# Kernel tuning notes

Measured on AMD Instinct MI355X. Metric: run time of the kernel, lower is better.

## Reference

```python
import jax, jax.numpy as jnp
import numpy as np

B, T, E = 65536, 50, 10


def _glorot(key, shape):
    fan_in, fan_out = shape[0], shape[-1]
    limit = np.sqrt(6.0 / (fan_in + fan_out))
    return jax.random.uniform(key, shape, jnp.float32, -limit, limit)


def setup_inputs() -> dict:
    key = jax.random.key(0)
    ks = jax.random.split(key, 20)
    inp = {
        "gru_hidden_state_inputs": jax.random.normal(ks[0], (B, T, E), jnp.float32),
        "attention_s": jax.random.uniform(ks[1], (B, T, E), jnp.float32),
        # initial hidden state: GlorotUniform(shape=(1, E)) as in the TF code
        "h0": _glorot(ks[2], (1, E)),
    }
    # R_t gate (sigmoid): input_w (with bias), hidden_w (no bias), Dense_sigmoid (with bias)
    inp["Wi_r"] = _glorot(ks[3], (E, E)); inp["bi_r"] = jnp.zeros((E,), jnp.float32)
    inp["Wh_r"] = _glorot(ks[4], (E, E))
    inp["Ws_r"] = _glorot(ks[5], (E, E)); inp["bs_r"] = jnp.zeros((E,), jnp.float32)
    # Z_t gate (sigmoid)
    inp["Wi_z"] = _glorot(ks[6], (E, E)); inp["bi_z"] = jnp.zeros((E,), jnp.float32)
    inp["Wh_z"] = _glorot(ks[7], (E, E))
    inp["Ws_z"] = _glorot(ks[8], (E, E)); inp["bs_z"] = jnp.zeros((E,), jnp.float32)
    # H_t_next candidate (tanh)
    inp["Wi_h"] = _glorot(ks[9], (E, E)); inp["bi_h"] = jnp.zeros((E,), jnp.float32)
    inp["Wh_h"] = _glorot(ks[10], (E, E))
    inp["Wt_h"] = _glorot(ks[11], (E, E)); inp["bt_h"] = jnp.zeros((E,), jnp.float32)
    return inp


def reference(gru_hidden_state_inputs, attention_s, h0,
              Wi_r, bi_r, Wh_r, Ws_r, bs_r,
              Wi_z, bi_z, Wh_z, Ws_z, bs_z,
              Wi_h, bi_h, Wh_h, Wt_h, bt_h):
    b, t, e = gru_hidden_state_inputs.shape
    h = jnp.broadcast_to(h0, (b, e))  # TF broadcasts the (1,E) init against the batch
    # scan over time: xs are [T, B, E]
    xs = (jnp.swapaxes(gru_hidden_state_inputs, 0, 1),
          jnp.swapaxes(attention_s, 0, 1))

    def step(h, xa):
        x_t, a_t = xa
        # note: each gate has an EXTRA dense layer (Dense_sigmoid / Dense_tanh are Dense layers)
        r = jax.nn.sigmoid((x_t @ Wi_r + bi_r + h @ Wh_r) @ Ws_r + bs_r)
        z = jax.nn.sigmoid((x_t @ Wi_z + bi_z + h @ Wh_z) @ Ws_z + bs_z)
        hc = jnp.tanh((x_t @ Wi_h + bi_h + (h * z) @ Wh_h) @ Wt_h + bt_h)
        Ra = a_t * r
        h_next = (1.0 - Ra) * h + Ra * hc
        return h_next, None

    h_final, _ = jax.lax.scan(step, h, xs)
    return h_final
```

## Files before the change

### kernel.cpp

```cpp
#include <hip/hip_runtime.h>

#define EDIM 10
#define TDIM 50
#define BATCH 65536
#define CWN 640

__device__ float g_cw[CWN];

typedef const __attribute__((address_space(4))) float cfloat;

__device__ __forceinline__ float fast_sigmoid(float x) {
    float e = __expf(-x);
    return __builtin_amdgcn_rcpf(1.0f + e);
}
__device__ __forceinline__ float fast_tanh(float x) {
    float e = __expf(2.0f * x);
    return 1.0f - 2.0f * __builtin_amdgcn_rcpf(e + 1.0f);
}

__global__ void collapse_weights(
    const float* __restrict__ Wi_r, const float* __restrict__ bi_r,
    const float* __restrict__ Wh_r, const float* __restrict__ Ws_r, const float* __restrict__ bs_r,
    const float* __restrict__ Wi_z, const float* __restrict__ bi_z,
    const float* __restrict__ Wh_z, const float* __restrict__ Ws_z, const float* __restrict__ bs_z,
    const float* __restrict__ Wi_h, const float* __restrict__ bi_h,
    const float* __restrict__ Wh_h, const float* __restrict__ Wt_h, const float* __restrict__ bt_h)
{
    for (int s = threadIdx.x; s < 630; s += 256) {
        int g, kind, k, e;
        if (s < 30)       { kind = 0; g = s / 10;      k = 0;                e = s % 10; }
        else if (s < 330) { kind = 1; int q = s - 30;  g = q / 100; k = (q % 100) / 10; e = q % 10; }
        else              { kind = 2; int q = s - 330; g = q / 100; k = (q % 100) / 10; e = q % 10; }
        const float* Wi = (g == 0) ? Wi_r : (g == 1) ? Wi_z : Wi_h;
        const float* Wh = (g == 0) ? Wh_r : (g == 1) ? Wh_z : Wh_h;
        const float* Ws = (g == 0) ? Ws_r : (g == 1) ? Ws_z : Wt_h;
        const float* bi = (g == 0) ? bi_r : (g == 1) ? bi_z : bi_h;
        const float* bs = (g == 0) ? bs_r : (g == 1) ? bs_z : bt_h;
        float v = 0.0f;
        if (kind == 0) {
            v = bs[e];
            #pragma unroll
            for (int j = 0; j < 10; j++) v += bi[j] * Ws[j * 10 + e];
        } else {
            const float* M = (kind == 1) ? Wi : Wh;
            #pragma unroll
            for (int j = 0; j < 10; j++) v += M[k * 10 + j] * Ws[j * 10 + e];
        }
        g_cw[s] = v;
    }
}

__global__ __launch_bounds__(256, 1) void augru_main(
    const float* __restrict__ x_all, const float* __restrict__ a_all,
    const float* __restrict__ h0,
    float* __restrict__ out)
{
    const int row = blockIdx.x * 256 + threadIdx.x;

    cfloat* cw = (cfloat*)(uintptr_t)(const float*)g_cw;

    const float2* xp = (const float2*)(x_all + (size_t)row * (TDIM * EDIM));
    const float2* ap = (const float2*)(a_all + (size_t)row * (TDIM * EDIM));

    float h[10];
    #pragma unroll
    for (int j = 0; j < 10; j++) h[j] = h0[j];

    float xc[10], ac[10];
    #pragma unroll
    for (int i = 0; i < 5; i++) {
        float2 v = xp[i]; xc[2 * i] = v.x; xc[2 * i + 1] = v.y;
        float2 u = ap[i]; ac[2 * i] = u.x; ac[2 * i + 1] = u.y;
    }

    int sofs = 0;

    #pragma unroll 1
    for (int t = 0; t < TDIM; t++) {
        asm volatile("" : "+s"(sofs));
        cfloat* w = cw + sofs;

        int tn = (t < TDIM - 1) ? (t + 1) : t;
        float xn[10], an[10];
        #pragma unroll
        for (int i = 0; i < 5; i++) {
            float2 v = xp[tn * 5 + i]; xn[2 * i] = v.x; xn[2 * i + 1] = v.y;
            float2 u = ap[tn * 5 + i]; an[2 * i] = u.x; an[2 * i + 1] = u.y;
        }

        float ur[10], uz[10], uh[10];
        #pragma unroll
        for (int j = 0; j < 10; j++) {
            ur[j] = w[j]; uz[j] = w[10 + j]; uh[j] = w[20 + j];
        }

        #pragma unroll
        for (int k = 0; k < 10; k++) {
            float xk = xc[k];
            #pragma unroll
            for (int j = 0; j < 10; j++) ur[j] = fmaf(xk, w[30 + k * 10 + j], ur[j]);
        }
        #pragma unroll
        for (int k = 0; k < 10; k++) {
            float xk = xc[k];
            #pragma unroll
            for (int j = 0; j < 10; j++) uz[j] = fmaf(xk, w[130 + k * 10 + j], uz[j]);
        }
        #pragma unroll
        for (int k = 0; k < 10; k++) {
            float hk = h[k];
            #pragma unroll
            for (int j = 0; j < 10; j++) ur[j] = fmaf(hk, w[330 + k * 10 + j], ur[j]);
        }
        #pragma unroll
        for (int k = 0; k < 10; k++) {
            float hk = h[k];
            #pragma unroll
            for (int j = 0; j < 10; j++) uz[j] = fmaf(hk, w[430 + k * 10 + j], uz[j]);
        }
        #pragma unroll
        for (int k = 0; k < 10; k++) {
            float xk = xc[k];
            #pragma unroll
            for (int j = 0; j < 10; j++) uh[j] = fmaf(xk, w[230 + k * 10 + j], uh[j]);
        }

        float hz[10];
        #pragma unroll
        for (int j = 0; j < 10; j++) hz[j] = h[j] * fast_sigmoid(uz[j]);

        #pragma unroll
        for (int k = 0; k < 10; k++) {
            float hk = hz[k];
            #pragma unroll
            for (int j = 0; j < 10; j++) uh[j] = fmaf(hk, w[530 + k * 10 + j], uh[j]);
        }

        #pragma unroll
        for (int j = 0; j < 10; j++) {
            float r  = fast_sigmoid(ur[j]);
            float hc = fast_tanh(uh[j]);
            float Ra = ac[j] * r;
            h[j] = fmaf(Ra, hc - h[j], h[j]);
        }

        #pragma unroll
        for (int j = 0; j < 10; j++) { xc[j] = xn[j]; ac[j] = an[j]; }
    }

    float2* orow = (float2*)(out + (size_t)row * EDIM);
    #pragma unroll
    for (int i = 0; i < 5; i++) orow[i] = make_float2(h[2 * i], h[2 * i + 1]);
}

extern "C" void kernel_launch(void* const* d_in, const int* in_sizes, int n_in,
                              void* d_out, int out_size, void* d_ws, size_t ws_size,
                              hipStream_t stream) {
    collapse_weights<<<1, 256, 0, stream>>>(
        (const float*)d_in[3],  (const float*)d_in[4],  (const float*)d_in[5],
        (const float*)d_in[6],  (const float*)d_in[7],
        (const float*)d_in[8],  (const float*)d_in[9],  (const float*)d_in[10],
        (const float*)d_in[11], (const float*)d_in[12],
        (const float*)d_in[13], (const float*)d_in[14], (const float*)d_in[15],
        (const float*)d_in[16], (const float*)d_in[17]);
    augru_main<<<BATCH / 256, 256, 0, stream>>>(
        (const float*)d_in[0], (const float*)d_in[1], (const float*)d_in[2],
        (float*)d_out);
}
```

Before: 353.8 us.

## Stage collapsed weights in LDS with padded rows and vector broadcast reads

Moves the collapsed weight matrix from scalar constant loads (s_load through the scalar cache) into shared memory, with each row padded to 12 floats so it can be read with float4/float2 LDS broadcast loads. Before, the weights came in through SGPR scalar loads, which are cheap and uniform. Now every lane issues LDS reads, so LDS instruction traffic and VGPR use go up in exchange for not depending on the scalar cache. The weight offset is also pinned to a VGPR instead of an SGPR.

```diff
diff --git a/kernel.cpp b/kernel.cpp
--- a/kernel.cpp
+++ b/kernel.cpp
@@ -3,11 +3,14 @@
 #define EDIM 10
 #define TDIM 50
 #define BATCH 65536
-#define CWN 640
+#define WPAD 12
+#define WTOT (63 * WPAD)
 
-__device__ float g_cw[CWN];
+__device__ float g_cwp[WTOT];
 
-typedef const __attribute__((address_space(4))) float cfloat;
+#define WROWA(g, k) (((g) * 20 + (k)) * WPAD)
+#define WROWB(g, k) (((g) * 20 + 10 + (k)) * WPAD)
+#define WBIAS(g)    ((60 + (g)) * WPAD)
 
 __device__ __forceinline__ float fast_sigmoid(float x) {
     float e = __expf(-x);
@@ -18,6 +21,28 @@
     return 1.0f - 2.0f * __builtin_amdgcn_rcpf(e + 1.0f);
 }
 
+#define MV_ROW(dst, s, rowptr) do {                                          \
+    const float* rp_ = (rowptr);                                             \
+    float4 w0_ = *(const float4*)(rp_);                                      \
+    float4 w1_ = *(const float4*)(rp_ + 4);                                  \
+    float2 w2_ = *(const float2*)(rp_ + 8);                                  \
+    dst[0] = fmaf((s), w0_.x, dst[0]); dst[1] = fmaf((s), w0_.y, dst[1]);    \
+    dst[2] = fmaf((s), w0_.z, dst[2]); dst[3] = fmaf((s), w0_.w, dst[3]);    \
+    dst[4] = fmaf((s), w1_.x, dst[4]); dst[5] = fmaf((s), w1_.y, dst[5]);    \
+    dst[6] = fmaf((s), w1_.z, dst[6]); dst[7] = fmaf((s), w1_.w, dst[7]);    \
+    dst[8] = fmaf((s), w2_.x, dst[8]); dst[9] = fmaf((s), w2_.y, dst[9]);    \
+} while (0)
+
+#define LD_ROW(dst, rowptr) do {                                             \
+    const float* rp_ = (rowptr);                                             \
+    float4 w0_ = *(const float4*)(rp_);                                      \
+    float4 w1_ = *(const float4*)(rp_ + 4);                                  \
+    float2 w2_ = *(const float2*)(rp_ + 8);                                  \
+    dst[0] = w0_.x; dst[1] = w0_.y; dst[2] = w0_.z; dst[3] = w0_.w;          \
+    dst[4] = w1_.x; dst[5] = w1_.y; dst[6] = w1_.z; dst[7] = w1_.w;          \
+    dst[8] = w2_.x; dst[9] = w2_.y;                                          \
+} while (0)
+
 __global__ void collapse_weights(
     const float* __restrict__ Wi_r, const float* __restrict__ bi_r,
     const float* __restrict__ Wh_r, const float* __restrict__ Ws_r, const float* __restrict__ bs_r,
@@ -26,27 +51,29 @@
     const float* __restrict__ Wi_h, const float* __restrict__ bi_h,
     const float* __restrict__ Wh_h, const float* __restrict__ Wt_h, const float* __restrict__ bt_h)
 {
-    for (int s = threadIdx.x; s < 630; s += 256) {
-        int g, kind, k, e;
-        if (s < 30)       { kind = 0; g = s / 10;      k = 0;                e = s % 10; }
-        else if (s < 330) { kind = 1; int q = s - 30;  g = q / 100; k = (q % 100) / 10; e = q % 10; }
-        else              { kind = 2; int q = s - 330; g = q / 100; k = (q % 100) / 10; e = q % 10; }
-        const float* Wi = (g == 0) ? Wi_r : (g == 1) ? Wi_z : Wi_h;
-        const float* Wh = (g == 0) ? Wh_r : (g == 1) ? Wh_z : Wh_h;
-        const float* Ws = (g == 0) ? Ws_r : (g == 1) ? Ws_z : Wt_h;
-        const float* bi = (g == 0) ? bi_r : (g == 1) ? bi_z : bi_h;
-        const float* bs = (g == 0) ? bs_r : (g == 1) ? bs_z : bt_h;
+    for (int s = threadIdx.x; s < WTOT; s += 256) {
+        int r = s / WPAD, j = s % WPAD;
         float v = 0.0f;
-        if (kind == 0) {
-            v = bs[e];
-            #pragma unroll
-            for (int j = 0; j < 10; j++) v += bi[j] * Ws[j * 10 + e];
-        } else {
-            const float* M = (kind == 1) ? Wi : Wh;
-            #pragma unroll
-            for (int j = 0; j < 10; j++) v += M[k * 10 + j] * Ws[j * 10 + e];
+        if (j < 10) {
+            if (r < 60) {
+                int g = r / 20, kind = (r % 20) / 10, k = r % 10;
+                const float* Ws = (g == 0) ? Ws_r : (g == 1) ? Ws_z : Wt_h;
+                const float* M  = (kind == 0)
+                    ? ((g == 0) ? Wi_r : (g == 1) ? Wi_z : Wi_h)
+                    : ((g == 0) ? Wh_r : (g == 1) ? Wh_z : Wh_h);
+                #pragma unroll
+                for (int jj = 0; jj < 10; jj++) v += M[k * 10 + jj] * Ws[jj * 10 + j];
+            } else {
+                int g = r - 60;
+                const float* Ws = (g == 0) ? Ws_r : (g == 1) ? Ws_z : Wt_h;
+                const float* bi = (g == 0) ? bi_r : (g == 1) ? bi_z : bi_h;
+                const float* bs = (g == 0) ? bs_r : (g == 1) ? bs_z : bt_h;
+                v = bs[j];
+                #pragma unroll
+                for (int jj = 0; jj < 10; jj++) v += bi[jj] * Ws[jj * 10 + j];
+            }
         }
-        g_cw[s] = v;
+        g_cwp[s] = v;
     }
 }
 
@@ -55,9 +82,11 @@
     const float* __restrict__ h0,
     float* __restrict__ out)
 {
+    __shared__ __align__(16) float WL[WTOT];
+    for (int s = threadIdx.x; s < WTOT; s += 256) WL[s] = g_cwp[s];
+    __syncthreads();
+
     const int row = blockIdx.x * 256 + threadIdx.x;
-
-    cfloat* cw = (cfloat*)(uintptr_t)(const float*)g_cw;
 
     const float2* xp = (const float2*)(x_all + (size_t)row * (TDIM * EDIM));
     const float2* ap = (const float2*)(a_all + (size_t)row * (TDIM * EDIM));
@@ -73,12 +102,12 @@
         float2 u = ap[i]; ac[2 * i] = u.x; ac[2 * i + 1] = u.y;
     }
 
-    int sofs = 0;
+    int wofs = 0;
 
     #pragma unroll 1
     for (int t = 0; t < TDIM; t++) {
-        asm volatile("" : "+s"(sofs));
-        cfloat* w = cw + sofs;
+        asm volatile("" : "+v"(wofs));
+        const float* w = (const float*)WL + wofs;
 
         int tn = (t < TDIM - 1) ? (t + 1) : t;
         float xn[10], an[10];
@@ -89,52 +118,27 @@
         }
 
         float ur[10], uz[10], uh[10];
-        #pragma unroll
-        for (int j = 0; j < 10; j++) {
-            ur[j] = w[j]; uz[j] = w[10 + j]; uh[j] = w[20 + j];
-        }
+        LD_ROW(ur, w + WBIAS(0));
+        LD_ROW(uz, w + WBIAS(1));
+        LD_ROW(uh, w + WBIAS(2));
 
         #pragma unroll
-        for (int k = 0; k < 10; k++) {
-            float xk = xc[k];
-            #pragma unroll
-            for (int j = 0; j < 10; j++) ur[j] = fmaf(xk, w[30 + k * 10 + j], ur[j]);
-        }
+        for (int k = 0; k < 10; k++) MV_ROW(ur, xc[k], w + WROWA(0, k));
         #pragma unroll
-        for (int k = 0; k < 10; k++) {
-            float xk = xc[k];
-            #pragma unroll
-            for (int j = 0; j < 10; j++) uz[j] = fmaf(xk, w[130 + k * 10 + j], uz[j]);
-        }
+        for (int k = 0; k < 10; k++) MV_ROW(uz, xc[k], w + WROWA(1, k));
         #pragma unroll
-        for (int k = 0; k < 10; k++) {
-            float hk = h[k];
-            #pragma unroll
-            for (int j = 0; j < 10; j++) ur[j] = fmaf(hk, w[330 + k * 10 + j], ur[j]);
-        }
+        for (int k = 0; k < 10; k++) MV_ROW(ur, h[k],  w + WROWB(0, k));
         #pragma unroll
-        for (int k = 0; k < 10; k++) {
-            float hk = h[k];
-            #pragma unroll
-            for (int j = 0; j < 10; j++) uz[j] = fmaf(hk, w[430 + k * 10 + j], uz[j]);
-        }
+        for (int k = 0; k < 10; k++) MV_ROW(uz, h[k],  w + WROWB(1, k));
         #pragma unroll
-        for (int k = 0; k < 10; k++) {
-            float xk = xc[k];
-            #pragma unroll
-            for (int j = 0; j < 10; j++) uh[j] = fmaf(xk, w[230 + k * 10 + j], uh[j]);
-        }
+        for (int k = 0; k < 10; k++) MV_ROW(uh, xc[k], w + WROWA(2, k));
 
         float hz[10];
         #pragma unroll
         for (int j = 0; j < 10; j++) hz[j] = h[j] * fast_sigmoid(uz[j]);
 
         #pragma unroll
-        for (int k = 0; k < 10; k++) {
-            float hk = hz[k];
-            #pragma unroll
-            for (int j = 0; j < 10; j++) uh[j] = fmaf(hk, w[530 + k * 10 + j], uh[j]);
-        }
+        for (int k = 0; k < 10; k++) MV_ROW(uh, hz[k], w + WROWB(2, k));
 
         #pragma unroll
         for (int j = 0; j < 10; j++) {
```

Result: slower. 367.3 us (+3.8%).

## Hold collapsed weights in registers: hidden weights in VGPRs, input weights via readlane

Applied to the files above, without the earlier changes.

Splits the collapsed weight table into an input/bias part and a hidden part. The hidden-weight matrices are loaded once into a large per-thread register array, and the input weights plus biases are spread across six per-lane registers and broadcast with readlane each step. The aim is to remove the repeated scalar constant loads of weights from the timestep loop. In exchange it sharply raises VGPR usage and adds hundreds of readlane instructions per step on the vector pipe.

```diff
diff --git a/kernel.cpp b/kernel.cpp
--- a/kernel.cpp
+++ b/kernel.cpp
@@ -3,11 +3,9 @@
 #define EDIM 10
 #define TDIM 50
 #define BATCH 65536
-#define CWN 640
-
-__device__ float g_cw[CWN];
-
-typedef const __attribute__((address_space(4))) float cfloat;
+
+__device__ __align__(16) float g_cwA[384];
+__device__ __align__(16) float g_cwB[304];
 
 __device__ __forceinline__ float fast_sigmoid(float x) {
     float e = __expf(-x);
@@ -17,6 +15,11 @@
     float e = __expf(2.0f * x);
     return 1.0f - 2.0f * __builtin_amdgcn_rcpf(e + 1.0f);
 }
+
+#define RL(i) __uint_as_float(__builtin_amdgcn_readlane( \
+                  __float_as_uint(wreg[(i) >> 6]), (i) & 63))
+#define FENCEW() asm volatile("" : "+v"(wreg[0]), "+v"(wreg[1]), "+v"(wreg[2]), \
+    "+v"(wreg[3]), "+v"(wreg[4]), "+v"(wreg[5]))
 
 __global__ void collapse_weights(
     const float* __restrict__ Wi_r, const float* __restrict__ bi_r,
@@ -26,27 +29,35 @@
     const float* __restrict__ Wi_h, const float* __restrict__ bi_h,
     const float* __restrict__ Wh_h, const float* __restrict__ Wt_h, const float* __restrict__ bt_h)
 {
-    for (int s = threadIdx.x; s < 630; s += 256) {
-        int g, kind, k, e;
-        if (s < 30)       { kind = 0; g = s / 10;      k = 0;                e = s % 10; }
-        else if (s < 330) { kind = 1; int q = s - 30;  g = q / 100; k = (q % 100) / 10; e = q % 10; }
-        else              { kind = 2; int q = s - 330; g = q / 100; k = (q % 100) / 10; e = q % 10; }
-        const float* Wi = (g == 0) ? Wi_r : (g == 1) ? Wi_z : Wi_h;
-        const float* Wh = (g == 0) ? Wh_r : (g == 1) ? Wh_z : Wh_h;
-        const float* Ws = (g == 0) ? Ws_r : (g == 1) ? Ws_z : Wt_h;
-        const float* bi = (g == 0) ? bi_r : (g == 1) ? bi_z : bi_h;
-        const float* bs = (g == 0) ? bs_r : (g == 1) ? bs_z : bt_h;
+    for (int s = threadIdx.x; s < 384; s += 256) {
         float v = 0.0f;
-        if (kind == 0) {
-            v = bs[e];
-            #pragma unroll
-            for (int j = 0; j < 10; j++) v += bi[j] * Ws[j * 10 + e];
-        } else {
-            const float* M = (kind == 1) ? Wi : Wh;
-            #pragma unroll
-            for (int j = 0; j < 10; j++) v += M[k * 10 + j] * Ws[j * 10 + e];
-        }
-        g_cw[s] = v;
+        if (s < 300) {
+            int g = s / 100, k = (s % 100) / 10, j = s % 10;
+            const float* Wi = (g == 0) ? Wi_r : (g == 1) ? Wi_z : Wi_h;
+            const float* Ws = (g == 0) ? Ws_r : (g == 1) ? Ws_z : Wt_h;
+            #pragma unroll
+            for (int jj = 0; jj < 10; jj++) v += Wi[k * 10 + jj] * Ws[jj * 10 + j];
+        } else if (s < 330) {
+            int g = (s - 300) / 10, j = (s - 300) % 10;
+            const float* Ws = (g == 0) ? Ws_r : (g == 1) ? Ws_z : Wt_h;
+            const float* bi = (g == 0) ? bi_r : (g == 1) ? bi_z : bi_h;
+            const float* bs = (g == 0) ? bs_r : (g == 1) ? bs_z : bt_h;
+            v = bs[j];
+            #pragma unroll
+            for (int jj = 0; jj < 10; jj++) v += bi[jj] * Ws[jj * 10 + j];
+        }
+        g_cwA[s] = v;
+    }
+    for (int s = threadIdx.x; s < 304; s += 256) {
+        float v = 0.0f;
+        if (s < 300) {
+            int g = s / 100, k = (s % 100) / 10, j = s % 10;
+            const float* Wh = (g == 0) ? Wh_r : (g == 1) ? Wh_z : Wh_h;
+            const float* Ws = (g == 0) ? Ws_r : (g == 1) ? Ws_z : Wt_h;
+            #pragma unroll
+            for (int jj = 0; jj < 10; jj++) v += Wh[k * 10 + jj] * Ws[jj * 10 + j];
+        }
+        g_cwB[s] = v;
     }
 }
 
@@ -55,9 +66,29 @@
     const float* __restrict__ h0,
     float* __restrict__ out)
 {
-    const int row = blockIdx.x * 256 + threadIdx.x;
-
-    cfloat* cw = (cfloat*)(uintptr_t)(const float*)g_cw;
+    const int lane = threadIdx.x & 63;
+    const int row  = blockIdx.x * 256 + threadIdx.x;
+
+    float wreg[6];
+    {
+        int lofs = 0;
+        asm volatile("" : "+v"(lofs));
+        #pragma unroll
+        for (int i = 0; i < 6; i++) wreg[i] = g_cwA[i * 64 + lane + lofs];
+    }
+
+    float Bv[300];
+    {
+        int lofs = 0;
+        asm volatile("" : "+v"(lofs));
+        const float* bp = (const float*)g_cwB + lofs;
+        #pragma unroll
+        for (int i = 0; i < 75; i++) {
+            float4 v = *(const float4*)(bp + 4 * i);
+            Bv[4 * i + 0] = v.x; Bv[4 * i + 1] = v.y;
+            Bv[4 * i + 2] = v.z; Bv[4 * i + 3] = v.w;
+        }
+    }
 
     const float2* xp = (const float2*)(x_all + (size_t)row * (TDIM * EDIM));
     const float2* ap = (const float2*)(a_all + (size_t)row * (TDIM * EDIM));
@@ -73,13 +104,8 @@
         float2 u = ap[i]; ac[2 * i] = u.x; ac[2 * i + 1] = u.y;
     }
 
-    int sofs = 0;
-
     #pragma unroll 1
     for (int t = 0; t < TDIM; t++) {
-        asm volatile("" : "+s"(sofs));
-        cfloat* w = cw + sofs;
-
         int tn = (t < TDIM - 1) ? (t + 1) : t;
         float xn[10], an[10];
         #pragma unroll
@@ -89,40 +115,45 @@
         }
 
         float ur[10], uz[10], uh[10];
+        FENCEW();
         #pragma unroll
         for (int j = 0; j < 10; j++) {
-            ur[j] = w[j]; uz[j] = w[10 + j]; uh[j] = w[20 + j];
-        }
-
+            ur[j] = RL(300 + j); uz[j] = RL(310 + j); uh[j] = RL(320 + j);
+        }
+
+        FENCEW();
         #pragma unroll
         for (int k = 0; k < 10; k++) {
             float xk = xc[k];
             #pragma unroll
-            for (int j = 0; j < 10; j++) ur[j] = fmaf(xk, w[30 + k * 10 + j], ur[j]);
-        }
+            for (int j = 0; j < 10; j++) ur[j] = fmaf(xk, RL(0 + k * 10 + j), ur[j]);
+        }
+        FENCEW();
         #pragma unroll
         for (int k = 0; k < 10; k++) {
             float xk = xc[k];
             #pragma unroll
-            for (int j = 0; j < 10; j++) uz[j] = fmaf(xk, w[130 + k * 10 + j], uz[j]);
-        }
+            for (int j = 0; j < 10; j++) uz[j] = fmaf(xk, RL(100 + k * 10 + j), uz[j]);
+        }
+        FENCEW();
+        #pragma unroll
+        for (int k = 0; k < 10; k++) {
+            float xk = xc[k];
+            #pragma unroll
+            for (int j = 0; j < 10; j++) uh[j] = fmaf(xk, RL(200 + k * 10 + j), uh[j]);
+        }
+
         #pragma unroll
         for (int k = 0; k < 10; k++) {
             float hk = h[k];
             #pragma unroll
-            for (int j = 0; j < 10; j++) ur[j] = fmaf(hk, w[330 + k * 10 + j], ur[j]);
+            for (int j = 0; j < 10; j++) ur[j] = fmaf(hk, Bv[0 + k * 10 + j], ur[j]);
         }
         #pragma unroll
         for (int k = 0; k < 10; k++) {
             float hk = h[k];
             #pragma unroll
-            for (int j = 0; j < 10; j++) uz[j] = fmaf(hk, w[430 + k * 10 + j], uz[j]);
-        }
-        #pragma unroll
-        for (int k = 0; k < 10; k++) {
-            float xk = xc[k];
-            #pragma unroll
-            for (int j = 0; j < 10; j++) uh[j] = fmaf(xk, w[230 + k * 10 + j], uh[j]);
+            for (int j = 0; j < 10; j++) uz[j] = fmaf(hk, Bv[100 + k * 10 + j], uz[j]);
         }
 
         float hz[10];
@@ -133,7 +164,7 @@
         for (int k = 0; k < 10; k++) {
             float hk = hz[k];
             #pragma unroll
-            for (int j = 0; j < 10; j++) uh[j] = fmaf(hk, w[530 + k * 10 + j], uh[j]);
+            for (int j = 0; j < 10; j++) uh[j] = fmaf(hk, Bv[200 + k * 10 + j], uh[j]);
         }
 
         #pragma unroll
```

Result: slower. 370.8 us (+4.8%).

## Split each batch row across four lanes with register-resident weight slices

Applied to the files above, without the earlier changes.

Each batch row is now handled by four lanes, each owning three output columns. Each lane keeps its slice of the collapsed weights in registers instead of reading scalar-constant memory, and the full hidden state and h*z vectors are exchanged with ds_bpermute every step. This raises the thread count fourfold and cuts per-thread FMA work, aiming at better latency hiding on the serial recurrence. In exchange it adds cross-lane permute traffic, does redundant x loads in all four lanes, and pads columns to 12, which wastes 2 of 12 columns of compute.

```diff
diff --git a/kernel.cpp b/kernel.cpp
--- a/kernel.cpp
+++ b/kernel.cpp
@@ -3,11 +3,11 @@
 #define EDIM 10
 #define TDIM 50
 #define BATCH 65536
-#define CWN 640
+#define CPL 3
 
-__device__ float g_cw[CWN];
-
-typedef const __attribute__((address_space(4))) float cfloat;
+__device__ __align__(16) float g_A[3][10][12];
+__device__ __align__(16) float g_B[3][10][12];
+__device__ __align__(16) float g_b[3][12];
 
 __device__ __forceinline__ float fast_sigmoid(float x) {
     float e = __expf(-x);
@@ -26,131 +26,158 @@
     const float* __restrict__ Wi_h, const float* __restrict__ bi_h,
     const float* __restrict__ Wh_h, const float* __restrict__ Wt_h, const float* __restrict__ bt_h)
 {
-    for (int s = threadIdx.x; s < 630; s += 256) {
-        int g, kind, k, e;
-        if (s < 30)       { kind = 0; g = s / 10;      k = 0;                e = s % 10; }
-        else if (s < 330) { kind = 1; int q = s - 30;  g = q / 100; k = (q % 100) / 10; e = q % 10; }
-        else              { kind = 2; int q = s - 330; g = q / 100; k = (q % 100) / 10; e = q % 10; }
-        const float* Wi = (g == 0) ? Wi_r : (g == 1) ? Wi_z : Wi_h;
-        const float* Wh = (g == 0) ? Wh_r : (g == 1) ? Wh_z : Wh_h;
-        const float* Ws = (g == 0) ? Ws_r : (g == 1) ? Ws_z : Wt_h;
-        const float* bi = (g == 0) ? bi_r : (g == 1) ? bi_z : bi_h;
-        const float* bs = (g == 0) ? bs_r : (g == 1) ? bs_z : bt_h;
+    for (int s = threadIdx.x; s < 756; s += 256) {
         float v = 0.0f;
-        if (kind == 0) {
-            v = bs[e];
-            #pragma unroll
-            for (int j = 0; j < 10; j++) v += bi[j] * Ws[j * 10 + e];
+        if (s < 720) {
+            int kind = s / 360;
+            int q = s % 360;
+            int g = q / 120, k = (q % 120) / 12, j = q % 12;
+            if (j < 10) {
+                const float* Ws = (g == 0) ? Ws_r : (g == 1) ? Ws_z : Wt_h;
+                const float* M  = (kind == 0)
+                    ? ((g == 0) ? Wi_r : (g == 1) ? Wi_z : Wi_h)
+                    : ((g == 0) ? Wh_r : (g == 1) ? Wh_z : Wh_h);
+                #pragma unroll
+                for (int jj = 0; jj < 10; jj++) v += M[k * 10 + jj] * Ws[jj * 10 + j];
+            }
+            if (kind == 0) g_A[g][k][j] = v; else g_B[g][k][j] = v;
         } else {
-            const float* M = (kind == 1) ? Wi : Wh;
-            #pragma unroll
-            for (int j = 0; j < 10; j++) v += M[k * 10 + j] * Ws[j * 10 + e];
+            int q = s - 720;
+            int g = q / 12, j = q % 12;
+            if (j < 10) {
+                const float* Ws = (g == 0) ? Ws_r : (g == 1) ? Ws_z : Wt_h;
+                const float* bi = (g == 0) ? bi_r : (g == 1) ? bi_z : bi_h;
+                const float* bs = (g == 0) ? bs_r : (g == 1) ? bs_z : bt_h;
+                v = bs[j];
+                #pragma unroll
+                for (int jj = 0; jj < 10; jj++) v += bi[jj] * Ws[jj * 10 + j];
+            }
+            g_b[g][j] = v;
         }
-        g_cw[s] = v;
     }
 }
 
-__global__ __launch_bounds__(256, 1) void augru_main(
+__global__ __launch_bounds__(256, 2) void augru_main(
     const float* __restrict__ x_all, const float* __restrict__ a_all,
     const float* __restrict__ h0,
     float* __restrict__ out)
 {
-    const int row = blockIdx.x * 256 + threadIdx.x;
+    const int lane = threadIdx.x & 63;
+    const int wv   = threadIdx.x >> 6;
+    const int q    = lane & 3;
+    const int rl   = lane >> 2;
+    const int row  = (blockIdx.x * 4 + wv) * 16 + rl;
+    const int c0   = q * CPL;
 
-    cfloat* cw = (cfloat*)(uintptr_t)(const float*)g_cw;
-
-    const float2* xp = (const float2*)(x_all + (size_t)row * (TDIM * EDIM));
-    const float2* ap = (const float2*)(a_all + (size_t)row * (TDIM * EDIM));
-
-    float h[10];
+    float wA[3][10][CPL], wB[3][10][CPL], wb[3][CPL];
     #pragma unroll
-    for (int j = 0; j < 10; j++) h[j] = h0[j];
-
-    float xc[10], ac[10];
-    #pragma unroll
-    for (int i = 0; i < 5; i++) {
-        float2 v = xp[i]; xc[2 * i] = v.x; xc[2 * i + 1] = v.y;
-        float2 u = ap[i]; ac[2 * i] = u.x; ac[2 * i + 1] = u.y;
+    for (int g = 0; g < 3; g++) {
+        #pragma unroll
+        for (int k = 0; k < 10; k++)
+            #pragma unroll
+            for (int j = 0; j < CPL; j++) {
+                wA[g][k][j] = g_A[g][k][c0 + j];
+                wB[g][k][j] = g_B[g][k][c0 + j];
+            }
+        #pragma unroll
+        for (int j = 0; j < CPL; j++) wb[g][j] = g_b[g][c0 + j];
     }
 
-    int sofs = 0;
+    const float2* xp2 = (const float2*)(x_all + (size_t)row * (TDIM * EDIM));
+    const float*  ap  = a_all + (size_t)row * (TDIM * EDIM);
+
+    int aco[CPL];
+    #pragma unroll
+    for (int j = 0; j < CPL; j++) aco[j] = (c0 + j < 10) ? (c0 + j) : 9;
+
+    float hown[CPL];
+    #pragma unroll
+    for (int j = 0; j < CPL; j++) hown[j] = h0[aco[j]];
+
+    const int pbase = (lane & ~3) * 4;
+
+    float xc[10], acv[CPL];
+    #pragma unroll
+    for (int i = 0; i < 5; i++) { float2 v = xp2[i]; xc[2 * i] = v.x; xc[2 * i + 1] = v.y; }
+    #pragma unroll
+    for (int j = 0; j < CPL; j++) acv[j] = ap[aco[j]];
 
     #pragma unroll 1
     for (int t = 0; t < TDIM; t++) {
-        asm volatile("" : "+s"(sofs));
-        cfloat* w = cw + sofs;
+        float hf[10];
+        #pragma unroll
+        for (int k = 0; k < 10; k++)
+            hf[k] = __int_as_float(__builtin_amdgcn_ds_bpermute(
+                        pbase + (k / 3) * 4, __float_as_int(hown[k % 3])));
 
         int tn = (t < TDIM - 1) ? (t + 1) : t;
-        float xn[10], an[10];
+        float xn[10], an[CPL];
         #pragma unroll
         for (int i = 0; i < 5; i++) {
-            float2 v = xp[tn * 5 + i]; xn[2 * i] = v.x; xn[2 * i + 1] = v.y;
-            float2 u = ap[tn * 5 + i]; an[2 * i] = u.x; an[2 * i + 1] = u.y;
+            float2 v = xp2[tn * 5 + i]; xn[2 * i] = v.x; xn[2 * i + 1] = v.y;
         }
+        #pragma unroll
+        for (int j = 0; j < CPL; j++) an[j] = ap[tn * 10 + aco[j]];
 
-        float ur[10], uz[10], uh[10];
+        float ur[CPL], uz[CPL], uh[CPL];
         #pragma unroll
-        for (int j = 0; j < 10; j++) {
-            ur[j] = w[j]; uz[j] = w[10 + j]; uh[j] = w[20 + j];
-        }
+        for (int j = 0; j < CPL; j++) { ur[j] = wb[0][j]; uz[j] = wb[1][j]; uh[j] = wb[2][j]; }
 
         #pragma unroll
         for (int k = 0; k < 10; k++) {
             float xk = xc[k];
             #pragma unroll
-            for (int j = 0; j < 10; j++) ur[j] = fmaf(xk, w[30 + k * 10 + j], ur[j]);
+            for (int j = 0; j < CPL; j++) {
+                ur[j] = fmaf(xk, wA[0][k][j], ur[j]);
+                uz[j] = fmaf(xk, wA[1][k][j], uz[j]);
+                uh[j] = fmaf(xk, wA[2][k][j], uh[j]);
+            }
         }
         #pragma unroll
         for (int k = 0; k < 10; k++) {
-            float xk = xc[k];
+            float hk = hf[k];
             #pragma unroll
-            for (int j = 0; j < 10; j++) uz[j] = fmaf(xk, w[130 + k * 10 + j], uz[j]);
-        }
-        #pragma unroll
-        for (int k = 0; k < 10; k++) {
-            float hk = h[k];
-            #pragma unroll
-            for (int j = 0; j < 10; j++) ur[j] = fmaf(hk, w[330 + k * 10 + j], ur[j]);
-        }
-        #pragma unroll
-        for (int k = 0; k < 10; k++) {
-            float hk = h[k];
-            #pragma unroll
-            for (int j = 0; j < 10; j++) uz[j] = fmaf(hk, w[430 + k * 10 + j], uz[j]);
-        }
-        #pragma unroll
-        for (int k = 0; k < 10; k++) {
-            float xk = xc[k];
-            #pragma unroll
-            for (int j = 0; j < 10; j++) uh[j] = fmaf(xk, w[230 + k * 10 + j], uh[j]);
+            for (int j = 0; j < CPL; j++) {
+                ur[j] = fmaf(hk, wB[0][k][j], ur[j]);
+                uz[j] = fmaf(hk, wB[1][k][j], uz[j]);
+            }
         }
 
-        float hz[10];
+        float hzo[CPL];
         #pragma unroll
-        for (int j = 0; j < 10; j++) hz[j] = h[j] * fast_sigmoid(uz[j]);
+        for (int j = 0; j < CPL; j++) hzo[j] = hown[j] * fast_sigmoid(uz[j]);
+
+        float hzf[10];
+        #pragma unroll
+        for (int k = 0; k < 10; k++)
+            hzf[k] = __int_as_float(__builtin_amdgcn_ds_bpermute(
+                         pbase + (k / 3) * 4, __float_as_int(hzo[k % 3])));
 
         #pragma unroll
         for (int k = 0; k < 10; k++) {
-            float hk = hz[k];
+            float hk = hzf[k];
             #pragma unroll
-            for (int j = 0; j < 10; j++) uh[j] = fmaf(hk, w[530 + k * 10 + j], uh[j]);
+            for (int j = 0; j < CPL; j++) uh[j] = fmaf(hk, wB[2][k][j], uh[j]);
         }
 
         #pragma unroll
-        for (int j = 0; j < 10; j++) {
+        for (int j = 0; j < CPL; j++) {
             float r  = fast_sigmoid(ur[j]);
             float hc = fast_tanh(uh[j]);
-            float Ra = ac[j] * r;
-            h[j] = fmaf(Ra, hc - h[j], h[j]);
+            float Ra = acv[j] * r;
+            hown[j] = fmaf(Ra, hc - hown[j], hown[j]);
         }
 
         #pragma unroll
-        for (int j = 0; j < 10; j++) { xc[j] = xn[j]; ac[j] = an[j]; }
+        for (int i = 0; i < 10; i++) xc[i] = xn[i];
+        #pragma unroll
+        for (int j = 0; j < CPL; j++) acv[j] = an[j];
     }
 
-    float2* orow = (float2*)(out + (size_t)row * EDIM);
+    float* orow = out + (size_t)row * EDIM;
     #pragma unroll
-    for (int i = 0; i < 5; i++) orow[i] = make_float2(h[2 * i], h[2 * i + 1]);
+    for (int j = 0; j < CPL; j++)
+        if (c0 + j < 10) orow[c0 + j] = hown[j];
 }
 
 extern "C" void kernel_launch(void* const* d_in, const int* in_sizes, int n_in,
@@ -163,7 +190,7 @@
         (const float*)d_in[11], (const float*)d_in[12],
         (const float*)d_in[13], (const float*)d_in[14], (const float*)d_in[15],
         (const float*)d_in[16], (const float*)d_in[17]);
-    augru_main<<<BATCH / 256, 256, 0, stream>>>(
+    augru_main<<<BATCH / 64, 256, 0, stream>>>(
         (const float*)d_in[0], (const float*)d_in[1], (const float*)d_in[2],
         (float*)d_out);
 }
```

Measured after the change: 603.2 us. +70.5%, slower.
